# Kernel optimization log

Measured on AMD Instinct MI355X. Metric: run time of the kernel, lower is better.

Reference implementation:

```python
import jax, jax.numpy as jnp
import numpy as np
from jax import lax


def setup_inputs() -> dict:
    key = jax.random.key(0)
    ks = jax.random.split(key, 5)
    B, N, F = 16, 2048, 64
    S, P, O = 4, 22, 42  # n_dimensions, n_propagate, n_filters
    x = jax.random.normal(ks[0], (B, N, F), dtype=jnp.float32)
    W_s = jax.random.normal(ks[1], (F, S), dtype=jnp.float32) * (1.0 / np.sqrt(F))
    b_s = jnp.zeros((S,), dtype=jnp.float32)
    W_f = jax.random.normal(ks[2], (F, P), dtype=jnp.float32) * (1.0 / np.sqrt(F))
    b_f = jnp.zeros((P,), dtype=jnp.float32)
    W_o = jax.random.normal(ks[3], (F + 2 * P, O), dtype=jnp.float32) * (1.0 / np.sqrt(F + 2 * P))
    b_o = jnp.zeros((O,), dtype=jnp.float32)
    return {"x": x, "W_s": W_s, "b_s": b_s, "W_f": W_f, "b_f": b_f,
            "W_o": W_o, "b_o": b_o, "n_neighbours": 40}


def reference(x, W_s, b_s, W_f, b_f, W_o, b_o, n_neighbours):
    # x: [B, N, F]
    coords = x @ W_s + b_s            # [B, N, S]   spatial transform
    feats = x @ W_f + b_f             # [B, N, P]   feature transform (FLR)
    # pairwise squared distances: [B, N, N]
    d2 = jnp.sum((coords[:, :, None, :] - coords[:, None, :, :]) ** 2, axis=-1)
    # k nearest (top_k of -distance); drop self (slot 0)
    neg_d, idx = lax.top_k(-d2, n_neighbours)        # [B, N, k]
    dist = -neg_d[:, :, 1:]                          # [B, N, k-1]
    nbr_idx = idx[:, :, 1:]                          # [B, N, k-1]
    weights = jnp.exp(-dist)[..., None]              # [B, N, k-1, 1]
    # batched gather of neighbour features: [B, N, k-1, P]
    nbr_feats = jax.vmap(lambda f, i: f[i])(feats, nbr_idx)
    weighted = nbr_feats * weights
    n_max = jnp.max(weighted, axis=2)                # [B, N, P]
    n_mean = jnp.mean(weighted, axis=2)              # [B, N, P]
    updated = jnp.concatenate([x, n_max, n_mean], axis=-1)  # [B, N, F+2P]
    return jnp.tanh(updated @ W_o + b_o)             # [B, N, n_filters]
```

## Files before the change

kernel.cpp:

```cpp
#include <hip/hip_runtime.h>
#include <math.h>

#define BB 16
#define NN 2048
#define FF 64
#define SS 4
#define PP 22
#define OO 42
#define FPDIM (FF + 2*PP)
#define NREG 32
#define XBLK 512
#define WST 68

__device__ __forceinline__ float readfirstlane_f32(float v) {
    return __uint_as_float((unsigned)__builtin_amdgcn_readfirstlane((int)__float_as_uint(v)));
}

__device__ __forceinline__ int wave_scan_dpp(int x) {
    x += __builtin_amdgcn_update_dpp(0, x, 0x111, 0xf, 0xf, true);
    x += __builtin_amdgcn_update_dpp(0, x, 0x112, 0xf, 0xf, true);
    x += __builtin_amdgcn_update_dpp(0, x, 0x114, 0xf, 0xf, true);
    x += __builtin_amdgcn_update_dpp(0, x, 0x118, 0xf, 0xf, true);
    x += __builtin_amdgcn_update_dpp(0, x, 0x142, 0xa, 0xf, true);
    x += __builtin_amdgcn_update_dpp(0, x, 0x143, 0xc, 0xf, true);
    return x;
}
__device__ __forceinline__ int wave_sum_dpp(int x) {
    return __builtin_amdgcn_readlane(wave_scan_dpp(x), 63);
}
__device__ __forceinline__ float wave_fsum_dpp(float x) {
    float t;
    t = __uint_as_float((unsigned)__builtin_amdgcn_update_dpp(0, (int)__float_as_uint(x), 0x111, 0xf, 0xf, true)); x += t;
    t = __uint_as_float((unsigned)__builtin_amdgcn_update_dpp(0, (int)__float_as_uint(x), 0x112, 0xf, 0xf, true)); x += t;
    t = __uint_as_float((unsigned)__builtin_amdgcn_update_dpp(0, (int)__float_as_uint(x), 0x114, 0xf, 0xf, true)); x += t;
    t = __uint_as_float((unsigned)__builtin_amdgcn_update_dpp(0, (int)__float_as_uint(x), 0x118, 0xf, 0xf, true)); x += t;
    t = __uint_as_float((unsigned)__builtin_amdgcn_update_dpp(0, (int)__float_as_uint(x), 0x142, 0xa, 0xf, true)); x += t;
    t = __uint_as_float((unsigned)__builtin_amdgcn_update_dpp(0, (int)__float_as_uint(x), 0x143, 0xc, 0xf, true)); x += t;
    return __uint_as_float((unsigned)__builtin_amdgcn_readlane((int)__float_as_uint(x), 63));
}

__global__ __launch_bounds__(256) void prep_kernel(
    const float* __restrict__ x, const float* __restrict__ Ws, const float* __restrict__ bs,
    const float* __restrict__ Wf, const float* __restrict__ bf,
    const float* __restrict__ Wo, const float* __restrict__ bo,
    float* __restrict__ coords, float* __restrict__ feats, float* __restrict__ xwo)
{
    __shared__ float wT[68 * WST];
    __shared__ float obufT[68 * WST];
    __shared__ float bvec[68];

    const int lane = threadIdx.x & 63;
    const int wv   = threadIdx.x >> 6;
    const int r0   = blockIdx.x * 64;

    const float4* xr = (const float4*)(x + (size_t)(r0 + lane) * FF);
    float4 xv[16];
    #pragma unroll
    for (int k4 = 0; k4 < 16; k4++) xv[k4] = xr[k4];

    {
        int t = threadIdx.x;
        int k = t >> 2, s = t & 3;
        wT[s * WST + k] = Ws[t];
    }
    for (int t = threadIdx.x; t < 64 * PP; t += 256) {
        int k = t / PP, c = t - k * PP;
        wT[(4 + c) * WST + k] = Wf[t];
    }
    for (int t = threadIdx.x; t < 64 * OO; t += 256) {
        int k = t / OO, o = t - k * OO;
        wT[(26 + o) * WST + k] = Wo[t];
    }
    if (threadIdx.x < 68) {
        int o = threadIdx.x;
        bvec[o] = o < 4 ? bs[o] : (o < 26 ? bf[o - 4] : bo[o - 26]);
    }
    __syncthreads();

    for (int u = 0; u < 17; u++) {
        int o = wv * 17 + u;
        float a0 = bvec[o], a1 = 0.f, a2 = 0.f, a3 = 0.f;
        const float4* wrow = (const float4*)(wT + o * WST);
        #pragma unroll
        for (int k4 = 0; k4 < 16; k4++) {
            float4 w4 = wrow[k4];
            a0 = fmaf(xv[k4].x, w4.x, a0);
            a1 = fmaf(xv[k4].y, w4.y, a1);
            a2 = fmaf(xv[k4].z, w4.z, a2);
            a3 = fmaf(xv[k4].w, w4.w, a3);
        }
        obufT[o * WST + lane] = (a0 + a1) + (a2 + a3);
    }
    __syncthreads();

    if (threadIdx.x < 64) {
        int r = threadIdx.x;
        float4 cv = make_float4(obufT[0 * WST + r], obufT[1 * WST + r],
                                obufT[2 * WST + r], obufT[3 * WST + r]);
        *((float4*)(coords + (size_t)(r0 + r) * SS)) = cv;
    }
    for (int t = threadIdx.x; t < 32 * PP; t += 256) {
        int row = t / 11, c2 = t - row * 11;
        float2 v = make_float2(obufT[(4 + 2 * c2) * WST + row],
                               obufT[(4 + 2 * c2 + 1) * WST + row]);
        *((float2*)(feats + (size_t)r0 * PP + 2 * t)) = v;
    }
    for (int t = threadIdx.x; t < 32 * OO; t += 256) {
        int row = t / 21, c2 = t - row * 21;
        float2 v = make_float2(obufT[(26 + 2 * c2) * WST + row],
                               obufT[(26 + 2 * c2 + 1) * WST + row]);
        *((float2*)(xwo + (size_t)r0 * OO + 2 * t)) = v;
    }
}

__global__ __launch_bounds__(128, 4) void knn_out_kernel(
    const float* __restrict__ coords, const float* __restrict__ feats,
    const float* __restrict__ xwo, const float* __restrict__ Wo,
    const int* __restrict__ nnbr, float* __restrict__ out)
{
    const int lane = threadIdx.x & 63;
    const int w    = threadIdx.x >> 6;
    const int q    = blockIdx.x * 2 + w;
    const int b    = q >> 11;
    const int i    = q & (NN - 1);

    int K = *nnbr; K = K < 2 ? 2 : (K > 64 ? 64 : K);

    __shared__ int   isel[2][64];
    __shared__ float wsel[2][64];
    __shared__ unsigned long long candk[2][64];
    __shared__ __align__(16) float urow[2][48];

    float xw = 0.f;
    if (lane < OO) xw = xwo[(size_t)q * OO + lane];

    const float4* cb = (const float4*)(coords + (size_t)b * NN * SS);
    float4 qv = cb[i];
    const float qx = readfirstlane_f32(qv.x);
    const float qy = readfirstlane_f32(qv.y);
    const float qz = readfirstlane_f32(qv.z);
    const float qw = readfirstlane_f32(qv.w);

    float d2r[NREG];
    float lmin = INFINITY;
    #pragma unroll 4
    for (int r = 0; r < NREG; r++) {
        float4 c = cb[r * 64 + lane];
        float d0 = qx - c.x, d1 = qy - c.y, d2 = qz - c.z, d3 = qw - c.w;
        float v = d0 * d0 + d1 * d1 + d2 * d2 + d3 * d3;
        d2r[r] = v;
        lmin = fminf(lmin, v);
    }

    float t0 = wave_fsum_dpp(lmin) * (1.0f / 64.0f);

    unsigned loU = 0u, hiU = 0x7F800000u;
    int cLo = 0, cHi = NN;
    int laneLo = 0, laneHi = NREG;
    float tPrev = t0; int cPrev = -1;

    if (t0 > 1e-30f) {
        float t1 = t0 * 0.75f, t2 = t0 * 0.95f, t3 = t0 * 1.15f, t4 = t0 * 1.40f;
        int l1 = 0, l2 = 0, l3 = 0, l4 = 0;
        #pragma unroll
        for (int r = 0; r < NREG; r++) {
            float v = d2r[r];
            l1 += (v < t1) ? 1 : 0;
            l2 += (v < t2) ? 1 : 0;
            l3 += (v < t3) ? 1 : 0;
            l4 += (v < t4) ? 1 : 0;
        }
        int s12 = wave_sum_dpp(l1 | (l2 << 16));
        int s34 = wave_sum_dpp(l3 | (l4 << 16));
        int c1 = s12 & 0xFFFF, c2 = s12 >> 16, c3 = s34 & 0xFFFF, c4 = s34 >> 16;
        if (c1 >= K)      { hiU = __float_as_uint(t1); cHi = c1; laneHi = l1; }
        else if (c2 >= K) { loU = __float_as_uint(t1); cLo = c1; laneLo = l1;
                            hiU = __float_as_uint(t2); cHi = c2; laneHi = l2; }
        else if (c3 >= K) { loU = __float_as_uint(t2); cLo = c2; laneLo = l2;
                            hiU = __float_as_uint(t3); cHi = c3; laneHi = l3; }
        else if (c4 >= K) { loU = __float_as_uint(t3); cLo = c3; laneLo = l3;
                            hiU = __float_as_uint(t4); cHi = c4; laneHi = l4; }
        else              { loU = __float_as_uint(t4); cLo = c4; laneLo = l4; }
        int bc = -1, bd = 0x7FFFFFFF; float bt = t0;
        int cs[4] = {c1, c2, c3, c4}; float ts[4] = {t1, t2, t3, t4};
        #pragma unroll
        for (int u = 0; u < 4; u++) {
            int d = cs[u] > K ? cs[u] - K : K - cs[u];
            if (cs[u] > 0 && d < bd) { bd = d; bc = cs[u]; bt = ts[u]; }
        }
        if (bc > 0) { tPrev = bt; cPrev = bc; }
        else        { tPrev = t4; cPrev = 0; }
    }

    int probes = 0;
    while (cHi - cLo > 64 && hiU - loU > 1u && probes < 20) {
        unsigned tAU = 0u, tBU = 0u;
        bool fell = false;
        if (cPrev > 0) {
            float g = tPrev * __fsqrt_rn((float)K / (float)cPrev);
            tAU = __float_as_uint(g * 0.88f); tBU = __float_as_uint(g * 1.18f);
        } else if (cPrev == 0) {
            tAU = __float_as_uint(tPrev * 3.0f); tBU = __float_as_uint(tPrev * 9.0f);
        } else fell = true;
        unsigned span = hiU - loU;
        if (fell || !(tAU > loU && tAU < hiU)) tAU = loU + span / 3u;
        if (tAU <= loU) tAU = loU + 1u;
        if (tAU >= hiU) tAU = hiU - 1u;
        if (fell || !(tBU >= tAU && tBU < hiU)) tBU = tAU + (hiU - tAU) / 2u;
        if (tBU < tAU) tBU = tAU;
        if (tBU >= hiU) tBU = hiU - 1u;

        float tA = __uint_as_float(tAU), tB = __uint_as_float(tBU);
        int clA = 0, clB = 0;
        #pragma unroll
        for (int r = 0; r < NREG; r++) {
            clA += (d2r[r] < tA) ? 1 : 0;
            clB += (d2r[r] < tB) ? 1 : 0;
        }
        int tot = wave_sum_dpp(clA | (clB << 16));
        int cA = tot & 0xFFFF, cB = tot >> 16;

        if (cA >= K) { hiU = tAU; cHi = cA; laneHi = clA; }
        else {
            loU = tAU; cLo = cA; laneLo = clA;
            if (cB >= K) { hiU = tBU; cHi = cB; laneHi = clB; }
            else         { loU = tBU; cLo = cB; laneLo = clB; }
        }
        int dA = cA > K ? cA - K : K - cA;
        int dB = cB > K ? cB - K : K - cB;
        if (cA > 0 && dA <= dB) { tPrev = tA; cPrev = cA; }
        else                    { tPrev = tB; cPrev = cB; }
        probes++;
    }

    const float lo = __uint_as_float(loU);
    const float hi = __uint_as_float(hiU);
    const int  need = K - cLo;

    int c1c = laneLo;
    int c2c = laneHi - laneLo;
    if (lane == (i & 63) && loU > 0u) c1c -= 1;
    int pk = c1c | (c2c << 16);
    int inc = wave_scan_dpp(pk);
    int excl = inc - pk;
    int tot  = __builtin_amdgcn_readlane(inc, 63);
    int b1 = excl & 0xFFFF;
    int b2 = excl >> 16;
    const int nbelow = tot & 0xFFFF;
    int ecand = tot >> 16; if (ecand > 64) ecand = 64;
    #pragma unroll
    for (int r = 0; r < NREG; r++) {
        float v = d2r[r];
        int j = r * 64 + lane;
        if ((v < lo) & (j != i)) { isel[w][b1] = j; wsel[w][b1] = v; b1++; }
        else if ((v >= lo) & (v < hi)) { if (b2 < 64) candk[w][b2] = ((unsigned long long)__float_as_uint(v) << 32) | (unsigned)j; b2++; }
    }
    __builtin_amdgcn_wave_barrier();

    int nsel;
    if (ecand == need && loU > 0u) {
        if (lane < ecand) {
            int slot = nbelow + lane;
            if (slot < 64) {
                unsigned long long k2 = candk[w][lane];
                isel[w][slot] = (int)(k2 & 0xFFFFFFFFull);
                wsel[w][slot] = __uint_as_float((unsigned)(k2 >> 32));
            }
        }
        nsel = nbelow + ecand;
        if (nsel > 64) nsel = 64;
    } else {
        unsigned long long mykey = ~0ull;
        if (lane < ecand) mykey = candk[w][lane];
        int mr = 0;
        for (int u = 0; u < ecand; u++) {
            unsigned long long k2 = candk[w][u];
            mr += (k2 < mykey) ? 1 : 0;
        }
        int mj = (int)(mykey & 0xFFFFFFFFull);
        bool ps = (lane < ecand) & (mr < need) & (mj != i);
        unsigned long long ms = __ballot(ps);
        if (ps) {
            int slot = nbelow + __popcll(ms & ((1ull << lane) - 1ull));
            if (slot < 64) { isel[w][slot] = mj; wsel[w][slot] = __uint_as_float((unsigned)(mykey >> 32)); }
        }
        nsel = nbelow + __popcll(ms);
        if (nsel > 64) nsel = 64;
    }
    __builtin_amdgcn_wave_barrier();
    if (lane < nsel) wsel[w][lane] = __expf(-wsel[w][lane]);
    __builtin_amdgcn_wave_barrier();

    const float* fb = feats + (size_t)b * NN * PP;
    int g = lane >> 5, c = lane & 31;
    float mx = -INFINITY, sm = 0.f;
    if (c < PP) {
        #pragma unroll 8
        for (int m = g; m < nsel; m += 2) {
            int j = isel[w][m]; float wt = wsel[w][m];
            float f = fb[(size_t)j * PP + c];
            float wf = wt * f;
            mx = fmaxf(mx, wf); sm += wf;
        }
    }
    float mx2 = __shfl_xor(mx, 32, 64);
    float sm2 = __shfl_xor(sm, 32, 64);
    mx = fmaxf(mx, mx2); sm += sm2;
    if (g == 0 && c < PP) {
        urow[w][c]      = mx;
        urow[w][PP + c] = sm / (float)(K - 1);
    }
    __builtin_amdgcn_wave_barrier();

    if (lane < OO) {
        float a0 = xw, a1 = 0.f, a2 = 0.f, a3 = 0.f;
        const float* wo = Wo + FF * OO + lane;
        #pragma unroll
        for (int k4 = 0; k4 < (2 * PP) / 4; k4++) {
            float4 u = *((const float4*)&urow[w][k4 * 4]);
            a0 = fmaf(u.x, wo[(k4 * 4 + 0) * OO], a0);
            a1 = fmaf(u.y, wo[(k4 * 4 + 1) * OO], a1);
            a2 = fmaf(u.z, wo[(k4 * 4 + 2) * OO], a2);
            a3 = fmaf(u.w, wo[(k4 * 4 + 3) * OO], a3);
        }
        float acc = (a0 + a1) + (a2 + a3);
        float a = acc < -12.f ? -12.f : (acc > 12.f ? 12.f : acc);
        float e2 = __expf(2.f * a);
        out[(size_t)q * OO + lane] = (e2 - 1.f) / (e2 + 1.f);
    }
}

extern "C" void kernel_launch(void* const* d_in, const int* in_sizes, int n_in,
                              void* d_out, int out_size, void* d_ws, size_t ws_size,
                              hipStream_t stream) {
    const float* x  = (const float*)d_in[0];
    const float* Ws = (const float*)d_in[1];
    const float* bs = (const float*)d_in[2];
    const float* Wf = (const float*)d_in[3];
    const float* bf = (const float*)d_in[4];
    const float* Wo = (const float*)d_in[5];
    const float* bo = (const float*)d_in[6];
    const int*   nn = (const int*)d_in[7];
    float* out = (float*)d_out;

    float* coords = (float*)d_ws;
    float* feats  = coords + (size_t)BB * NN * SS;
    float* xwo    = feats  + (size_t)BB * NN * PP;

    prep_kernel<<<XBLK, 256, 0, stream>>>(x, Ws, bs, Wf, bf, Wo, bo, coords, feats, xwo);
    knn_out_kernel<<<(BB * NN) / 2, 128, 0, stream>>>(coords, feats, xwo, Wo, nn, out);
}
```

Measured before the change: 171.3 us.

## Fuse prep and kNN stages into one cooperative kernel with grid sync

Replaces the two-kernel launch with one cooperative kernel. The first 512 blocks compute the coords/feats/xwo projections, a grid-wide sync follows, and then all 1024 blocks run the kNN/aggregation stage, each wave handling 8 queries. The goal is to remove the second launch and the gap between kernels, and to raise work per wave. It relies on all 1024 blocks being co-resident at 4 blocks per CU. If the cooperative launch fails, it falls back to the old two-kernel path.

```diff
diff --git a/kernel.cpp b/kernel.cpp
--- a/kernel.cpp
+++ b/kernel.cpp
@@ -1,5 +1,8 @@
 #include <hip/hip_runtime.h>
+#include <hip/hip_cooperative_groups.h>
 #include <math.h>
+
+namespace cg = cooperative_groups;
 
 #define BB 16
 #define NN 2048
@@ -7,15 +10,14 @@
 #define SS 4
 #define PP 22
 #define OO 42
-#define FPDIM (FF + 2*PP)
 #define NREG 32
-#define XBLK 512
+#define GRID 1024
+#define PTILES 512
 #define WST 68
 
 __device__ __forceinline__ float readfirstlane_f32(float v) {
     return __uint_as_float((unsigned)__builtin_amdgcn_readfirstlane((int)__float_as_uint(v)));
 }
-
 __device__ __forceinline__ int wave_scan_dpp(int x) {
     x += __builtin_amdgcn_update_dpp(0, x, 0x111, 0xf, 0xf, true);
     x += __builtin_amdgcn_update_dpp(0, x, 0x112, 0xf, 0xf, true);
@@ -37,6 +39,309 @@
     t = __uint_as_float((unsigned)__builtin_amdgcn_update_dpp(0, (int)__float_as_uint(x), 0x142, 0xa, 0xf, true)); x += t;
     t = __uint_as_float((unsigned)__builtin_amdgcn_update_dpp(0, (int)__float_as_uint(x), 0x143, 0xc, 0xf, true)); x += t;
     return __uint_as_float((unsigned)__builtin_amdgcn_readlane((int)__float_as_uint(x), 63));
+}
+
+__global__ __launch_bounds__(256, 4) void fused_kernel(
+    const float* __restrict__ x, const float* __restrict__ Ws, const float* __restrict__ bs,
+    const float* __restrict__ Wf, const float* __restrict__ bf,
+    const float* __restrict__ Wo, const float* __restrict__ bo,
+    const int* __restrict__ nnbr,
+    float* __restrict__ coords, float* __restrict__ feats, float* __restrict__ xwo,
+    float* __restrict__ out)
+{
+    __shared__ __align__(16) float smem[68 * WST + 68];
+
+    const int lane = threadIdx.x & 63;
+    const int wv   = threadIdx.x >> 6;
+
+    if (blockIdx.x < PTILES) {
+        float* wT   = smem;
+        float* bvec = smem + 68 * WST;
+        const int r0 = blockIdx.x * 64;
+
+        const float4* xr = (const float4*)(x + (size_t)(r0 + lane) * FF);
+        float4 xv[16];
+        #pragma unroll
+        for (int k4 = 0; k4 < 16; k4++) xv[k4] = xr[k4];
+
+        {
+            int t = threadIdx.x;
+            int k = t >> 2, s = t & 3;
+            wT[s * WST + k] = Ws[t];
+        }
+        for (int t = threadIdx.x; t < 64 * PP; t += 256) {
+            int k = t / PP, c = t - k * PP;
+            wT[(4 + c) * WST + k] = Wf[t];
+        }
+        for (int t = threadIdx.x; t < 64 * OO; t += 256) {
+            int k = t / OO, o = t - k * OO;
+            wT[(26 + o) * WST + k] = Wo[t];
+        }
+        if (threadIdx.x < 68) {
+            int o = threadIdx.x;
+            bvec[o] = o < 4 ? bs[o] : (o < 26 ? bf[o - 4] : bo[o - 26]);
+        }
+        __syncthreads();
+
+        float acc[17];
+        #pragma unroll
+        for (int u = 0; u < 17; u++) {
+            int o = wv * 17 + u;
+            float a0 = bvec[o], a1 = 0.f, a2 = 0.f, a3 = 0.f;
+            const float4* wrow = (const float4*)(wT + o * WST);
+            #pragma unroll
+            for (int k4 = 0; k4 < 16; k4++) {
+                float4 w4 = wrow[k4];
+                a0 = fmaf(xv[k4].x, w4.x, a0);
+                a1 = fmaf(xv[k4].y, w4.y, a1);
+                a2 = fmaf(xv[k4].z, w4.z, a2);
+                a3 = fmaf(xv[k4].w, w4.w, a3);
+            }
+            acc[u] = (a0 + a1) + (a2 + a3);
+        }
+        __syncthreads();
+
+        #pragma unroll
+        for (int u = 0; u < 17; u++)
+            smem[(wv * 17 + u) * WST + lane] = acc[u];
+        __syncthreads();
+
+        if (threadIdx.x < 64) {
+            int r = threadIdx.x;
+            float4 cv = make_float4(smem[0 * WST + r], smem[1 * WST + r],
+                                    smem[2 * WST + r], smem[3 * WST + r]);
+            *((float4*)(coords + (size_t)(r0 + r) * SS)) = cv;
+        }
+        for (int t = threadIdx.x; t < 32 * PP; t += 256) {
+            int row = t / 11, c2 = t - row * 11;
+            float2 v = make_float2(smem[(4 + 2 * c2) * WST + row],
+                                   smem[(4 + 2 * c2 + 1) * WST + row]);
+            *((float2*)(feats + (size_t)r0 * PP + 2 * t)) = v;
+        }
+        for (int t = threadIdx.x; t < 32 * OO; t += 256) {
+            int row = t / 21, c2 = t - row * 21;
+            float2 v = make_float2(smem[(26 + 2 * c2) * WST + row],
+                                   smem[(26 + 2 * c2 + 1) * WST + row]);
+            *((float2*)(xwo + (size_t)r0 * OO + 2 * t)) = v;
+        }
+    }
+
+    cg::this_grid().sync();
+
+    float* wbase = smem + 320 * wv;
+    unsigned long long* candk = (unsigned long long*)wbase;
+    float* urow = wbase + 128;
+    int*   isel = (int*)(wbase + 176);
+    float* wsel = wbase + 240;
+
+    int K = *nnbr; K = K < 2 ? 2 : (K > 64 ? 64 : K);
+
+    const int gw = blockIdx.x * 4 + wv;
+    const int b  = (gw * 8) >> 11;
+    const float4* cb = (const float4*)(coords + (size_t)b * NN * SS);
+    const float* fb = feats + (size_t)b * NN * PP;
+
+    for (int it = 0; it < 8; it++) {
+        const int q = gw * 8 + it;
+        const int i = q & (NN - 1);
+
+        float xw = 0.f;
+        if (lane < OO) xw = xwo[(size_t)q * OO + lane];
+
+        float4 qv = cb[i];
+        const float qx = readfirstlane_f32(qv.x);
+        const float qy = readfirstlane_f32(qv.y);
+        const float qz = readfirstlane_f32(qv.z);
+        const float qw = readfirstlane_f32(qv.w);
+
+        float d2r[NREG];
+        float lmin = INFINITY;
+        #pragma unroll 4
+        for (int r = 0; r < NREG; r++) {
+            float4 c = cb[r * 64 + lane];
+            float d0 = qx - c.x, d1 = qy - c.y, d2 = qz - c.z, d3 = qw - c.w;
+            float v = d0 * d0 + d1 * d1 + d2 * d2 + d3 * d3;
+            d2r[r] = v;
+            lmin = fminf(lmin, v);
+        }
+
+        float t0 = wave_fsum_dpp(lmin) * (1.0f / 64.0f);
+
+        unsigned loU = 0u, hiU = 0x7F800000u;
+        int cLo = 0, cHi = NN;
+        int laneLo = 0, laneHi = NREG;
+        float tPrev = t0; int cPrev = -1;
+
+        if (t0 > 1e-30f) {
+            float t1 = t0 * 0.75f, t2 = t0 * 0.95f, t3 = t0 * 1.15f, t4 = t0 * 1.40f;
+            int l1 = 0, l2 = 0, l3 = 0, l4 = 0;
+            #pragma unroll
+            for (int r = 0; r < NREG; r++) {
+                float v = d2r[r];
+                l1 += (v < t1) ? 1 : 0;
+                l2 += (v < t2) ? 1 : 0;
+                l3 += (v < t3) ? 1 : 0;
+                l4 += (v < t4) ? 1 : 0;
+            }
+            int s12 = wave_sum_dpp(l1 | (l2 << 16));
+            int s34 = wave_sum_dpp(l3 | (l4 << 16));
+            int c1 = s12 & 0xFFFF, c2 = s12 >> 16, c3 = s34 & 0xFFFF, c4 = s34 >> 16;
+            if (c1 >= K)      { hiU = __float_as_uint(t1); cHi = c1; laneHi = l1; }
+            else if (c2 >= K) { loU = __float_as_uint(t1); cLo = c1; laneLo = l1;
+                                hiU = __float_as_uint(t2); cHi = c2; laneHi = l2; }
+            else if (c3 >= K) { loU = __float_as_uint(t2); cLo = c2; laneLo = l2;
+                                hiU = __float_as_uint(t3); cHi = c3; laneHi = l3; }
+            else if (c4 >= K) { loU = __float_as_uint(t3); cLo = c3; laneLo = l3;
+                                hiU = __float_as_uint(t4); cHi = c4; laneHi = l4; }
+            else              { loU = __float_as_uint(t4); cLo = c4; laneLo = l4; }
+            int bc = -1, bd = 0x7FFFFFFF; float bt = t0;
+            int cs[4] = {c1, c2, c3, c4}; float ts[4] = {t1, t2, t3, t4};
+            #pragma unroll
+            for (int u = 0; u < 4; u++) {
+                int d = cs[u] > K ? cs[u] - K : K - cs[u];
+                if (cs[u] > 0 && d < bd) { bd = d; bc = cs[u]; bt = ts[u]; }
+            }
+            if (bc > 0) { tPrev = bt; cPrev = bc; }
+            else        { tPrev = t4; cPrev = 0; }
+        }
+
+        int probes = 0;
+        while (cHi - cLo > 64 && hiU - loU > 1u && probes < 20) {
+            unsigned tAU = 0u, tBU = 0u;
+            bool fell = false;
+            if (cPrev > 0) {
+                float g = tPrev * __fsqrt_rn((float)K / (float)cPrev);
+                tAU = __float_as_uint(g * 0.88f); tBU = __float_as_uint(g * 1.18f);
+            } else if (cPrev == 0) {
+                tAU = __float_as_uint(tPrev * 3.0f); tBU = __float_as_uint(tPrev * 9.0f);
+            } else fell = true;
+            unsigned span = hiU - loU;
+            if (fell || !(tAU > loU && tAU < hiU)) tAU = loU + span / 3u;
+            if (tAU <= loU) tAU = loU + 1u;
+            if (tAU >= hiU) tAU = hiU - 1u;
+            if (fell || !(tBU >= tAU && tBU < hiU)) tBU = tAU + (hiU - tAU) / 2u;
+            if (tBU < tAU) tBU = tAU;
+            if (tBU >= hiU) tBU = hiU - 1u;
+
+            float tA = __uint_as_float(tAU), tB = __uint_as_float(tBU);
+            int clA = 0, clB = 0;
+            #pragma unroll
+            for (int r = 0; r < NREG; r++) {
+                clA += (d2r[r] < tA) ? 1 : 0;
+                clB += (d2r[r] < tB) ? 1 : 0;
+            }
+            int tot = wave_sum_dpp(clA | (clB << 16));
+            int cA = tot & 0xFFFF, cB = tot >> 16;
+
+            if (cA >= K) { hiU = tAU; cHi = cA; laneHi = clA; }
+            else {
+                loU = tAU; cLo = cA; laneLo = clA;
+                if (cB >= K) { hiU = tBU; cHi = cB; laneHi = clB; }
+                else         { loU = tBU; cLo = cB; laneLo = clB; }
+            }
+            int dA = cA > K ? cA - K : K - cA;
+            int dB = cB > K ? cB - K : K - cB;
+            if (cA > 0 && dA <= dB) { tPrev = tA; cPrev = cA; }
+            else                    { tPrev = tB; cPrev = cB; }
+            probes++;
+        }
+
+        const float lo = __uint_as_float(loU);
+        const float hi = __uint_as_float(hiU);
+        const int  need = K - cLo;
+
+        int c1c = laneLo;
+        int c2c = laneHi - laneLo;
+        if (lane == (i & 63) && loU > 0u) c1c -= 1;
+        int pk = c1c | (c2c << 16);
+        int inc = wave_scan_dpp(pk);
+        int excl = inc - pk;
+        int tot  = __builtin_amdgcn_readlane(inc, 63);
+        int b1 = excl & 0xFFFF;
+        int b2 = excl >> 16;
+        const int nbelow = tot & 0xFFFF;
+        int ecand = tot >> 16; if (ecand > 64) ecand = 64;
+        #pragma unroll
+        for (int r = 0; r < NREG; r++) {
+            float v = d2r[r];
+            int j = r * 64 + lane;
+            if ((v < lo) & (j != i)) { isel[b1] = j; wsel[b1] = v; b1++; }
+            else if ((v >= lo) & (v < hi)) { if (b2 < 64) candk[b2] = ((unsigned long long)__float_as_uint(v) << 32) | (unsigned)j; b2++; }
+        }
+        __builtin_amdgcn_wave_barrier();
+
+        int nsel;
+        if (ecand == need && loU > 0u) {
+            if (lane < ecand) {
+                int slot = nbelow + lane;
+                if (slot < 64) {
+                    unsigned long long k2 = candk[lane];
+                    isel[slot] = (int)(k2 & 0xFFFFFFFFull);
+                    wsel[slot] = __uint_as_float((unsigned)(k2 >> 32));
+                }
+            }
+            nsel = nbelow + ecand;
+            if (nsel > 64) nsel = 64;
+        } else {
+            unsigned long long mykey = ~0ull;
+            if (lane < ecand) mykey = candk[lane];
+            int mr = 0;
+            for (int u = 0; u < ecand; u++) {
+                unsigned long long k2 = candk[u];
+                mr += (k2 < mykey) ? 1 : 0;
+            }
+            int mj = (int)(mykey & 0xFFFFFFFFull);
+            bool ps = (lane < ecand) & (mr < need) & (mj != i);
+            unsigned long long ms = __ballot(ps);
+            if (ps) {
+                int slot = nbelow + __popcll(ms & ((1ull << lane) - 1ull));
+                if (slot < 64) { isel[slot] = mj; wsel[slot] = __uint_as_float((unsigned)(mykey >> 32)); }
+            }
+            nsel = nbelow + __popcll(ms);
+            if (nsel > 64) nsel = 64;
+        }
+        __builtin_amdgcn_wave_barrier();
+        if (lane < nsel) wsel[lane] = __expf(-wsel[lane]);
+        __builtin_amdgcn_wave_barrier();
+
+        int g = lane >> 5, c = lane & 31;
+        float mx = -INFINITY, sm = 0.f;
+        if (c < PP) {
+            #pragma unroll 8
+            for (int m = g; m < nsel; m += 2) {
+                int j = isel[m]; float wt = wsel[m];
+                float f = fb[(size_t)j * PP + c];
+                float wf = wt * f;
+                mx = fmaxf(mx, wf); sm += wf;
+            }
+        }
+        float mx2 = __shfl_xor(mx, 32, 64);
+        float sm2 = __shfl_xor(sm, 32, 64);
+        mx = fmaxf(mx, mx2); sm += sm2;
+        if (g == 0 && c < PP) {
+            urow[c]      = mx;
+            urow[PP + c] = sm / (float)(K - 1);
+        }
+        __builtin_amdgcn_wave_barrier();
+
+        if (lane < OO) {
+            float a0 = xw, a1 = 0.f, a2 = 0.f, a3 = 0.f;
+            const float* wo = Wo + FF * OO + lane;
+            #pragma unroll
+            for (int k4 = 0; k4 < (2 * PP) / 4; k4++) {
+                float4 u = *((const float4*)&urow[k4 * 4]);
+                a0 = fmaf(u.x, wo[(k4 * 4 + 0) * OO], a0);
+                a1 = fmaf(u.y, wo[(k4 * 4 + 1) * OO], a1);
+                a2 = fmaf(u.z, wo[(k4 * 4 + 2) * OO], a2);
+                a3 = fmaf(u.w, wo[(k4 * 4 + 3) * OO], a3);
+            }
+            float acc = (a0 + a1) + (a2 + a3);
+            float a = acc < -12.f ? -12.f : (acc > 12.f ? 12.f : acc);
+            float e2 = __expf(2.f * a);
+            out[(size_t)q * OO + lane] = (e2 - 1.f) / (e2 + 1.f);
+        }
+        __builtin_amdgcn_wave_barrier();
+    }
 }
 
 __global__ __launch_bounds__(256) void prep_kernel(
@@ -347,6 +652,14 @@
     float* feats  = coords + (size_t)BB * NN * SS;
     float* xwo    = feats  + (size_t)BB * NN * PP;
 
-    prep_kernel<<<XBLK, 256, 0, stream>>>(x, Ws, bs, Wf, bf, Wo, bo, coords, feats, xwo);
-    knn_out_kernel<<<(BB * NN) / 2, 128, 0, stream>>>(coords, feats, xwo, Wo, nn, out);
-}
+    void* kargs[] = { (void*)&x, (void*)&Ws, (void*)&bs, (void*)&Wf, (void*)&bf,
+                      (void*)&Wo, (void*)&bo, (void*)&nn,
+                      (void*)&coords, (void*)&feats, (void*)&xwo, (void*)&out };
+    hipError_t err = hipLaunchCooperativeKernel((void*)fused_kernel,
+                                                dim3(GRID), dim3(256),
+                                                kargs, 0, stream);
+    if (err != hipSuccess) {
+        prep_kernel<<<PTILES, 256, 0, stream>>>(x, Ws, bs, Wf, bf, Wo, bo, coords, feats, xwo);
+        knn_out_kernel<<<(BB * NN) / 2, 128, 0, stream>>>(coords, feats, xwo, Wo, nn, out);
+    }
+}
```

Result: slower. 457.1 us (+166.8%).

## Replace two-threshold bracketing search with single-threshold count search and full candidate rank

Applied to the files above, without the earlier changes.

Replaces the lo/hi bracketing search with a single-threshold search. It keeps guessing a cutoff, using sqrt-scaled guesses and then bisection, until between K and 64 points fall below it. All candidates below the cutoff are then ranked in one pass and the K nearest are kept. This removes the dual-threshold counting, the separate below/candidate compaction and the fast-path branch, which simplifies control flow. In exchange, each search step counts only one threshold, so convergence may take more iterations, and the final rank loop always covers up to 64 candidates.

```diff
diff --git a/kernel.cpp b/kernel.cpp
--- a/kernel.cpp
+++ b/kernel.cpp
@@ -7,7 +7,6 @@
 #define SS 4
 #define PP 22
 #define OO 42
-#define FPDIM (FF + 2*PP)
 #define NREG 32
 #define XBLK 512
 #define WST 68
@@ -24,9 +23,6 @@
     x += __builtin_amdgcn_update_dpp(0, x, 0x142, 0xa, 0xf, true);
     x += __builtin_amdgcn_update_dpp(0, x, 0x143, 0xc, 0xf, true);
     return x;
-}
-__device__ __forceinline__ int wave_sum_dpp(int x) {
-    return __builtin_amdgcn_readlane(wave_scan_dpp(x), 63);
 }
 __device__ __forceinline__ float wave_fsum_dpp(float x) {
     float t;
@@ -153,140 +149,75 @@
     }
 
     float t0 = wave_fsum_dpp(lmin) * (1.0f / 64.0f);
-
-    unsigned loU = 0u, hiU = 0x7F800000u;
-    int cLo = 0, cHi = NN;
-    int laneLo = 0, laneHi = NREG;
-    float tPrev = t0; int cPrev = -1;
-
-    if (t0 > 1e-30f) {
-        float t1 = t0 * 0.75f, t2 = t0 * 0.95f, t3 = t0 * 1.15f, t4 = t0 * 1.40f;
-        int l1 = 0, l2 = 0, l3 = 0, l4 = 0;
+    if (!(t0 > 1e-30f)) t0 = 1e-30f;
+
+    const float targetc = 0.5f * (float)(K + 64);
+    unsigned bLoU = 0u;
+    unsigned bHiU = 0x7F800000u;
+    unsigned hiU  = __float_as_uint(t0 * __fsqrt_rn(targetc * (1.0f / 40.0f)));
+    if (hiU <= bLoU) hiU = bLoU + 1u;
+    if (hiU >= bHiU) hiU = bHiU - 1u;
+
+    int ecand = 0, lcnt = 0, incl = 0;
+    for (int att = 0; att < 32; att++) {
+        float hi = __uint_as_float(hiU);
+        lcnt = 0;
         #pragma unroll
-        for (int r = 0; r < NREG; r++) {
-            float v = d2r[r];
-            l1 += (v < t1) ? 1 : 0;
-            l2 += (v < t2) ? 1 : 0;
-            l3 += (v < t3) ? 1 : 0;
-            l4 += (v < t4) ? 1 : 0;
-        }
-        int s12 = wave_sum_dpp(l1 | (l2 << 16));
-        int s34 = wave_sum_dpp(l3 | (l4 << 16));
-        int c1 = s12 & 0xFFFF, c2 = s12 >> 16, c3 = s34 & 0xFFFF, c4 = s34 >> 16;
-        if (c1 >= K)      { hiU = __float_as_uint(t1); cHi = c1; laneHi = l1; }
-        else if (c2 >= K) { loU = __float_as_uint(t1); cLo = c1; laneLo = l1;
-                            hiU = __float_as_uint(t2); cHi = c2; laneHi = l2; }
-        else if (c3 >= K) { loU = __float_as_uint(t2); cLo = c2; laneLo = l2;
-                            hiU = __float_as_uint(t3); cHi = c3; laneHi = l3; }
-        else if (c4 >= K) { loU = __float_as_uint(t3); cLo = c3; laneLo = l3;
-                            hiU = __float_as_uint(t4); cHi = c4; laneHi = l4; }
-        else              { loU = __float_as_uint(t4); cLo = c4; laneLo = l4; }
-        int bc = -1, bd = 0x7FFFFFFF; float bt = t0;
-        int cs[4] = {c1, c2, c3, c4}; float ts[4] = {t1, t2, t3, t4};
-        #pragma unroll
-        for (int u = 0; u < 4; u++) {
-            int d = cs[u] > K ? cs[u] - K : K - cs[u];
-            if (cs[u] > 0 && d < bd) { bd = d; bc = cs[u]; bt = ts[u]; }
-        }
-        if (bc > 0) { tPrev = bt; cPrev = bc; }
-        else        { tPrev = t4; cPrev = 0; }
-    }
-
-    int probes = 0;
-    while (cHi - cLo > 64 && hiU - loU > 1u && probes < 20) {
-        unsigned tAU = 0u, tBU = 0u;
-        bool fell = false;
-        if (cPrev > 0) {
-            float g = tPrev * __fsqrt_rn((float)K / (float)cPrev);
-            tAU = __float_as_uint(g * 0.88f); tBU = __float_as_uint(g * 1.18f);
-        } else if (cPrev == 0) {
-            tAU = __float_as_uint(tPrev * 3.0f); tBU = __float_as_uint(tPrev * 9.0f);
-        } else fell = true;
-        unsigned span = hiU - loU;
-        if (fell || !(tAU > loU && tAU < hiU)) tAU = loU + span / 3u;
-        if (tAU <= loU) tAU = loU + 1u;
-        if (tAU >= hiU) tAU = hiU - 1u;
-        if (fell || !(tBU >= tAU && tBU < hiU)) tBU = tAU + (hiU - tAU) / 2u;
-        if (tBU < tAU) tBU = tAU;
-        if (tBU >= hiU) tBU = hiU - 1u;
-
-        float tA = __uint_as_float(tAU), tB = __uint_as_float(tBU);
-        int clA = 0, clB = 0;
-        #pragma unroll
-        for (int r = 0; r < NREG; r++) {
-            clA += (d2r[r] < tA) ? 1 : 0;
-            clB += (d2r[r] < tB) ? 1 : 0;
-        }
-        int tot = wave_sum_dpp(clA | (clB << 16));
-        int cA = tot & 0xFFFF, cB = tot >> 16;
-
-        if (cA >= K) { hiU = tAU; cHi = cA; laneHi = clA; }
-        else {
-            loU = tAU; cLo = cA; laneLo = clA;
-            if (cB >= K) { hiU = tBU; cHi = cB; laneHi = clB; }
-            else         { loU = tBU; cLo = cB; laneLo = clB; }
-        }
-        int dA = cA > K ? cA - K : K - cA;
-        int dB = cB > K ? cB - K : K - cB;
-        if (cA > 0 && dA <= dB) { tPrev = tA; cPrev = cA; }
-        else                    { tPrev = tB; cPrev = cB; }
-        probes++;
-    }
-
-    const float lo = __uint_as_float(loU);
+        for (int r = 0; r < NREG; r++) lcnt += (d2r[r] < hi) ? 1 : 0;
+        incl  = wave_scan_dpp(lcnt);
+        ecand = __builtin_amdgcn_readlane(incl, 63);
+        if (ecand >= K && ecand <= 64) break;
+
+        unsigned prop;
+        if (ecand < K) {
+            bLoU = hiU;
+            float denom = (float)(ecand < 2 ? 2 : ecand);
+            float sc = __fsqrt_rn(targetc / denom);
+            sc = sc > 4.0f ? 4.0f : sc;
+            prop = __float_as_uint(hi * sc);
+        } else {
+            bHiU = hiU;
+            prop = __float_as_uint(hi * __fsqrt_rn(targetc / (float)ecand));
+        }
+        if (bHiU - bLoU <= 1u) break;
+        if (att >= 3 || !(prop > bLoU && prop < bHiU))
+            prop = bLoU + ((bHiU - bLoU) >> 1);
+        if (prop <= bLoU) prop = bLoU + 1u;
+        if (prop >= bHiU) prop = bHiU - 1u;
+        hiU = prop;
+    }
     const float hi = __uint_as_float(hiU);
-    const int  need = K - cLo;
-
-    int c1c = laneLo;
-    int c2c = laneHi - laneLo;
-    if (lane == (i & 63) && loU > 0u) c1c -= 1;
-    int pk = c1c | (c2c << 16);
-    int inc = wave_scan_dpp(pk);
-    int excl = inc - pk;
-    int tot  = __builtin_amdgcn_readlane(inc, 63);
-    int b1 = excl & 0xFFFF;
-    int b2 = excl >> 16;
-    const int nbelow = tot & 0xFFFF;
-    int ecand = tot >> 16; if (ecand > 64) ecand = 64;
+    if (ecand > 64) ecand = 64;
+
+    int b2 = incl - lcnt;
     #pragma unroll
     for (int r = 0; r < NREG; r++) {
         float v = d2r[r];
-        int j = r * 64 + lane;
-        if ((v < lo) & (j != i)) { isel[w][b1] = j; wsel[w][b1] = v; b1++; }
-        else if ((v >= lo) & (v < hi)) { if (b2 < 64) candk[w][b2] = ((unsigned long long)__float_as_uint(v) << 32) | (unsigned)j; b2++; }
-    }
-    __builtin_amdgcn_wave_barrier();
-
-    int nsel;
-    if (ecand == need && loU > 0u) {
-        if (lane < ecand) {
-            int slot = nbelow + lane;
-            if (slot < 64) {
-                unsigned long long k2 = candk[w][lane];
-                isel[w][slot] = (int)(k2 & 0xFFFFFFFFull);
-                wsel[w][slot] = __uint_as_float((unsigned)(k2 >> 32));
-            }
-        }
-        nsel = nbelow + ecand;
-        if (nsel > 64) nsel = 64;
-    } else {
-        unsigned long long mykey = ~0ull;
-        if (lane < ecand) mykey = candk[w][lane];
-        int mr = 0;
-        for (int u = 0; u < ecand; u++) {
-            unsigned long long k2 = candk[w][u];
-            mr += (k2 < mykey) ? 1 : 0;
-        }
-        int mj = (int)(mykey & 0xFFFFFFFFull);
-        bool ps = (lane < ecand) & (mr < need) & (mj != i);
-        unsigned long long ms = __ballot(ps);
-        if (ps) {
-            int slot = nbelow + __popcll(ms & ((1ull << lane) - 1ull));
-            if (slot < 64) { isel[w][slot] = mj; wsel[w][slot] = __uint_as_float((unsigned)(mykey >> 32)); }
-        }
-        nsel = nbelow + __popcll(ms);
-        if (nsel > 64) nsel = 64;
-    }
+        if (v < hi) {
+            if (b2 < 64)
+                candk[w][b2] = ((unsigned long long)__float_as_uint(v) << 32) | (unsigned)(r * 64 + lane);
+            b2++;
+        }
+    }
+    __builtin_amdgcn_wave_barrier();
+
+    unsigned long long mykey = ~0ull;
+    if (lane < ecand) mykey = candk[w][lane];
+    int mr = 0;
+    for (int u = 0; u < ecand; u++) {
+        unsigned long long ku = candk[w][u];
+        mr += (ku < mykey) ? 1 : 0;
+    }
+    int mj = (int)(mykey & 0xFFFFFFFFull);
+    bool ps = (lane < ecand) & (mr < K) & (mj != i);
+    unsigned long long ms = __ballot(ps);
+    if (ps) {
+        int slot = __popcll(ms & ((1ull << lane) - 1ull));
+        isel[w][slot] = mj;
+        wsel[w][slot] = __uint_as_float((unsigned)(mykey >> 32));
+    }
+    int nsel = __popcll(ms);
+    if (nsel > 64) nsel = 64;
     __builtin_amdgcn_wave_barrier();
     if (lane < nsel) wsel[w][lane] = __expf(-wsel[w][lane]);
     __builtin_amdgcn_wave_barrier();
```

Measured after the change: 163.3 us. 4.7% less time.
